# Kernel optimization log

Measured on AMD Instinct MI355X. Metric: run time of the kernel, lower is better.

## Reference

```python
import jax, jax.numpy as jnp
import numpy as np

B, S, H, W, L = 32, 512, 768, 256, 8  # batch, subword seq, hidden, max words, max group size
INTENT, SLOT = 26, 121


def setup_inputs() -> dict:
    key = jax.random.key(0)
    ks = jax.random.split(key, 16)
    sc = 0.02
    res_all = jax.random.normal(ks[0], (B, S, H), jnp.float32)
    res = jax.random.normal(ks[1], (B, H), jnp.float32)
    # group covers indices start..start+lens inclusive (lens+1 <= L elements)
    token_start_idxs = jax.random.randint(ks[2], (B, W), 0, S - L, jnp.int32)
    subword_lengths = jax.random.randint(ks[3], (B, W), 1, L, jnp.int32)  # 1..7
    return {
        'res_all': res_all,
        'res': res,
        'token_start_idxs': token_start_idxs,
        'subword_lengths': subword_lengths,
        'Wsq_w': jax.random.normal(ks[4], (H, H), jnp.float32) * sc,
        'Wsq_b': jnp.zeros((H,), jnp.float32),
        'Wsk_w': jax.random.normal(ks[5], (H, H), jnp.float32) * sc,
        'Wsk_b': jnp.zeros((H,), jnp.float32),
        'Wsv_w': jax.random.normal(ks[6], (H, H), jnp.float32) * sc,
        'Wsv_b': jnp.zeros((H,), jnp.float32),
        'lin_id_w': jax.random.normal(ks[7], (INTENT, H), jnp.float32) * sc,
        'lin_id_b': jnp.zeros((INTENT,), jnp.float32),
        'lin_slot_w': jax.random.normal(ks[8], (SLOT, H), jnp.float32) * sc,
        'lin_slot_b': jnp.zeros((SLOT,), jnp.float32),
    }


def reference(res_all, res, token_start_idxs, subword_lengths,
              Wsq_w, Wsq_b, Wsk_w, Wsk_b, Wsv_w, Wsv_b,
              lin_id_w, lin_id_b, lin_slot_w, lin_slot_b):
    # intent head on pooled output
    res_id = res @ lin_id_w.T + lin_id_b  # [B, INTENT]

    # gather padded subword groups: torch.range is inclusive -> lens+1 subwords
    offs = jnp.arange(L, dtype=jnp.int32)                        # [L]
    idx = token_start_idxs[:, :, None] + offs[None, None, :]     # [B, W, L]
    idx = jnp.clip(idx, 0, S - 1)
    group = res_all[jnp.arange(B)[:, None, None], idx]           # [B, W, L, H]
    valid = offs[None, None, :] <= subword_lengths[:, :, None]   # [B, W, L], lens+1 valid

    # SAA_Attn: only the first row's attention output is used
    q0 = group[:, :, 0, :] @ Wsq_w.T + Wsq_b                     # [B, W, H]
    K = group @ Wsk_w.T + Wsk_b                                  # [B, W, L, H]
    V = group @ Wsv_w.T + Wsv_b                                  # [B, W, L, H]
    scores = jnp.einsum('bwh,bwkh->bwk', q0, K)                  # [B, W, L]
    scores = jnp.where(valid, scores, jnp.float32(-1e9))
    attn = jax.nn.softmax(scores, axis=-1)
    first = group[:, :, 0, :]
    attn_word = jnp.einsum('bwk,bwkh->bwh', attn, V) + first     # [B, W, H]

    # lens == 1 branch bypasses attention entirely
    word = jnp.where((subword_lengths == 1)[:, :, None], first, attn_word)

    res_sf = word @ lin_slot_w.T + lin_slot_b                    # [B, W, SLOT]
    return res_id, res_sf
```

## Files before the change

### kernel.cpp

```cpp
#include <hip/hip_runtime.h>
#include <cstdint>
#include <cstddef>

#define BB 32
#define SS 512
#define HH 768
#define WW 256
#define LL 8
#define NINTENT 26
#define NSLOT 121

typedef float f32x4 __attribute__((ext_vector_type(4)));
typedef __bf16 bf16x8 __attribute__((ext_vector_type(8)));

static __device__ __forceinline__ float bf2f(unsigned short u) {
    union { unsigned int i; float f; } x; x.i = ((unsigned int)u) << 16; return x.f;
}
static __device__ __forceinline__ unsigned short f2bf(float f) {
    union { float f; unsigned int i; } x; x.f = f;
    unsigned int r = (x.i + 0x7fffu + ((x.i >> 16) & 1u)) >> 16;
    return (unsigned short)r;
}

static __device__ __forceinline__ void gload16(const void* g, void* l) {
    __builtin_amdgcn_global_load_lds(
        (const __attribute__((address_space(1))) void*)g,
        (__attribute__((address_space(3))) void*)l, 16, 0, 0);
}

#define MF(a, b, c) __builtin_amdgcn_mfma_f32_16x16x32_bf16((a), (b), (c), 0, 0, 0)

__global__ __launch_bounds__(256) void prep_w(
    const float* __restrict__ Wk, const float* __restrict__ Wq,
    const float* __restrict__ Wv, const float* __restrict__ Ws,
    const float* __restrict__ bq, const float* __restrict__ bv,
    unsigned short* __restrict__ WkT_hi, unsigned short* __restrict__ WkT_lo,
    unsigned short* __restrict__ WqT_hi, unsigned short* __restrict__ WqT_lo,
    unsigned short* __restrict__ WvT, unsigned short* __restrict__ Wcomb,
    float* __restrict__ u_part,
    float* __restrict__ wsbv_part)
{
    int bid = blockIdx.x;
    int t = threadIdx.x;

    if (bid < 432) {
        __shared__ float tl[64][65];
        int mb = bid / 144, tb = bid % 144;
        int tx = tb % 12, ty = tb / 12;
        const float* src = (mb == 0) ? Wk : (mb == 1) ? Wq : Wv;
        int rr = t >> 4, c4 = (t & 15) * 4;
#pragma unroll
        for (int j = 0; j < 4; j++) {
            float4 v = *reinterpret_cast<const float4*>(
                &src[(size_t)(ty * 64 + rr + 16 * j) * HH + tx * 64 + c4]);
            tl[rr + 16 * j][c4 + 0] = v.x; tl[rr + 16 * j][c4 + 1] = v.y;
            tl[rr + 16 * j][c4 + 2] = v.z; tl[rr + 16 * j][c4 + 3] = v.w;
        }
        __syncthreads();
        int il = t >> 4, o4 = (t & 15) * 4;
        unsigned short* dhi = (mb == 0) ? WkT_hi : (mb == 1) ? WqT_hi : WvT;
        unsigned short* dlo = (mb == 0) ? WkT_lo : WqT_lo;
#pragma unroll
        for (int j = 0; j < 4; j++) {
            int i = il + 16 * j;
            float v0 = tl[o4 + 0][i], v1 = tl[o4 + 1][i];
            float v2 = tl[o4 + 2][i], v3 = tl[o4 + 3][i];
            size_t off = (size_t)(tx * 64 + i) * HH + ty * 64 + o4;
            ushort4 h;
            h.x = f2bf(v0); h.y = f2bf(v1); h.z = f2bf(v2); h.w = f2bf(v3);
            *reinterpret_cast<ushort4*>(&dhi[off]) = h;
            if (mb < 2) {
                ushort4 l;
                l.x = f2bf(v0 - bf2f(h.x)); l.y = f2bf(v1 - bf2f(h.y));
                l.z = f2bf(v2 - bf2f(h.z)); l.w = f2bf(v3 - bf2f(h.w));
                *reinterpret_cast<ushort4*>(&dlo[off]) = l;
            }
        }
        if (mb == 0) {
            int c = t >> 2, q = t & 3;
            float s = 0.f;
#pragma unroll
            for (int r = 0; r < 16; r++)
                s += bq[ty * 64 + q * 16 + r] * tl[q * 16 + r][c];
            s += __shfl_xor(s, 1);
            s += __shfl_xor(s, 2);
            if (q == 0) u_part[ty * HH + tx * 64 + c] = s;
        }
    } else {
        __shared__ float wred[4];
        int bid2 = bid - 432;
        int idx = bid2 * 256 + t;
        int row = idx / HH, col = idx % HH;
        float v = (row < NSLOT) ? Ws[row * HH + col] : 0.f;
        Wcomb[row * 1536 + col] = f2bf(v);
        float pv = v * bv[col];
        int lane = t & 63, wave = t >> 6;
#pragma unroll
        for (int off = 32; off > 0; off >>= 1) pv += __shfl_xor(pv, off);
        if (lane == 0) wred[wave] = pv;
        __syncthreads();
        if (t == 0)
            wsbv_part[(bid2 % 3) * 128 + row] = wred[0] + wred[1] + wred[2] + wred[3];
    }
}

__global__ __launch_bounds__(256) void gemm_weights(
    const uint4* __restrict__ WkT_hi, const uint4* __restrict__ WkT_lo,
    const uint4* __restrict__ WqT_hi, const uint4* __restrict__ WqT_lo,
    const uint4* __restrict__ WvT, const uint4* __restrict__ Wcomb,
    const float* __restrict__ res_all, const int* __restrict__ starts,
    const float* __restrict__ res, const float* __restrict__ id_w,
    const float* __restrict__ id_b,
    float* __restrict__ Ppart,
    float* __restrict__ WRpart,
    unsigned short* __restrict__ slotA,
    float* __restrict__ out)
{
    __shared__ uint4 sA[512];
    __shared__ uint4 sB[512];
    int bid = blockIdx.x;
    int t = threadIdx.x;
    int lane = t & 63, wave = t >> 6;

    if (bid >= 2384) {
        int w = (bid - 2384) * 4 + wave;
        int bb = w / 26, o = w - bb * 26;
        const float* rrow = res + bb * HH + lane * 12;
        const float* wrow = id_w + o * HH + lane * 12;
        float s = 0.f;
#pragma unroll
        for (int c = 0; c < 3; c++) {
            float4 a = *reinterpret_cast<const float4*>(&rrow[c * 4]);
            float4 b = *reinterpret_cast<const float4*>(&wrow[c * 4]);
            s += a.x * b.x + a.y * b.y + a.z * b.z + a.w * b.w;
        }
#pragma unroll
        for (int off = 32; off > 0; off >>= 1) s += __shfl_xor(s, off);
        if (lane == 0) out[bb * NINTENT + o] = s + id_b[o];
        return;
    }
    if (bid >= 336) {
        int gw = (bid - 336) * 4 + wave;
        int b = gw >> 8;
        int s0 = starts[gw];
        const float* src = res_all + (size_t)(b * SS + s0) * HH + lane * 12;
        unsigned short* dst = slotA + (size_t)gw * 1536 + lane * 12;
#pragma unroll
        for (int c2 = 0; c2 < 3; c2++) {
            float4 v = *reinterpret_cast<const float4*>(&src[c2 * 4]);
            ushort4 o;
            o.x = f2bf(v.x); o.y = f2bf(v.y); o.z = f2bf(v.z); o.w = f2bf(v.w);
            *reinterpret_cast<ushort4*>(&dst[c2 * 4]) = o;
        }
        return;
    }

    int wm = wave >> 1, wn = wave & 1;
    int l16 = lane & 15, lk = lane >> 4;
    int srow = lane >> 2, schk = lane & 3;
    uint4* sA0 = &sA[wave * 128];
    uint4* sA1 = &sA[wave * 128 + 64];
    uint4* sB0 = &sB[wave * 128];
    uint4* sB1 = &sB[wave * 128 + 64];

    f32x4 acc[4][4] = {};

    if (bid < 288) {
        int tile = bid >> 3, ks = bid & 7;
        int mt = tile / 6, nt = tile % 6;
        int kb = ks * 12;
#pragma unroll
        for (int p = 0; p < 3; p++) {
            const uint4* Ab = (p == 1) ? WkT_lo : WkT_hi;
            const uint4* Bb = (p == 2) ? WqT_lo : WqT_hi;
            const uint4* Ag0 = Ab + (size_t)(mt * 128 + wave * 32 + srow) * 96 + kb + schk;
            const uint4* Ag1 = Ag0 + (size_t)16 * 96;
            const uint4* Bg0 = Bb + (size_t)(nt * 128 + wave * 32 + srow) * 96 + kb + schk;
            const uint4* Bg1 = Bg0 + (size_t)16 * 96;
            for (int k0 = 0; k0 < 12; k0 += 4) {
                gload16(Ag0 + k0, sA0); gload16(Ag1 + k0, sA1);
                gload16(Bg0 + k0, sB0); gload16(Bg1 + k0, sB1);
                __syncthreads();
                bf16x8 af[4], bfr[4];
#pragma unroll
                for (int i = 0; i < 4; i++)
                    af[i] = *reinterpret_cast<const bf16x8*>(&sA[(wm * 64 + i * 16 + l16) * 4 + lk]);
#pragma unroll
                for (int j = 0; j < 4; j++)
                    bfr[j] = *reinterpret_cast<const bf16x8*>(&sB[(wn * 64 + j * 16 + l16) * 4 + lk]);
#pragma unroll
                for (int i = 0; i < 4; i++)
#pragma unroll
                    for (int j = 0; j < 4; j++)
                        acc[i][j] = MF(af[i], bfr[j], acc[i][j]);
                __syncthreads();
            }
        }
        float* dst = Ppart + (size_t)ks * 589824;
#pragma unroll
        for (int i = 0; i < 4; i++)
#pragma unroll
            for (int j = 0; j < 4; j++) {
                int col = nt * 128 + wn * 64 + j * 16 + l16;
#pragma unroll
                for (int q = 0; q < 4; q++) {
                    int row = mt * 128 + wm * 64 + i * 16 + lk * 4 + q;
                    dst[(size_t)row * HH + col] = acc[i][j][q];
                }
            }
    } else {
        int idx = bid - 288;
        int nt = idx >> 3, ks = idx & 7;
        int kb = ks * 12;
        const uint4* Ag0 = Wcomb + (size_t)(wave * 32 + srow) * 192 + kb + schk;
        const uint4* Ag1 = Ag0 + (size_t)16 * 192;
        const uint4* Bg0 = WvT + (size_t)(nt * 128 + wave * 32 + srow) * 96 + kb + schk;
        const uint4* Bg1 = Bg0 + (size_t)16 * 96;
        for (int k0 = 0; k0 < 12; k0 += 4) {
            gload16(Ag0 + k0, sA0); gload16(Ag1 + k0, sA1);
            gload16(Bg0 + k0, sB0); gload16(Bg1 + k0, sB1);
            __syncthreads();
            bf16x8 af[4], bfr[4];
#pragma unroll
            for (int i = 0; i < 4; i++)
                af[i] = *reinterpret_cast<const bf16x8*>(&sA[(wm * 64 + i * 16 + l16) * 4 + lk]);
#pragma unroll
            for (int j = 0; j < 4; j++)
                bfr[j] = *reinterpret_cast<const bf16x8*>(&sB[(wn * 64 + j * 16 + l16) * 4 + lk]);
#pragma unroll
            for (int i = 0; i < 4; i++)
#pragma unroll
                for (int j = 0; j < 4; j++)
                    acc[i][j] = MF(af[i], bfr[j], acc[i][j]);
            __syncthreads();
        }
        float* dst = WRpart + (size_t)ks * 98304;
#pragma unroll
        for (int i = 0; i < 4; i++)
#pragma unroll
            for (int j = 0; j < 4; j++) {
                int col = nt * 128 + wn * 64 + j * 16 + l16;
#pragma unroll
                for (int q = 0; q < 4; q++) {
                    int row = wm * 64 + i * 16 + lk * 4 + q;
                    dst[(size_t)row * HH + col] = acc[i][j][q];
                }
            }
    }
}

__global__ __launch_bounds__(256) void psum_kernel(
    const float4* __restrict__ Ppart, ushort4* __restrict__ Pb,
    const float4* __restrict__ WRpart, unsigned short* __restrict__ Wcomb,
    const float* __restrict__ u_part, float* __restrict__ u,
    const float* __restrict__ wsbv_part, float* __restrict__ wsbv)
{
    int bid = blockIdx.x, t = threadIdx.x;
    if (bid < 576) {
        int i = bid * 256 + t;
        float4 s = Ppart[i];
#pragma unroll
        for (int k = 1; k < 8; k++) {
            float4 v = Ppart[(size_t)k * 147456 + i];
            s.x += v.x; s.y += v.y; s.z += v.z; s.w += v.w;
        }
        ushort4 o;
        o.x = f2bf(s.x); o.y = f2bf(s.y); o.z = f2bf(s.z); o.w = f2bf(s.w);
        Pb[i] = o;
    } else if (bid < 672) {
        int q = (bid - 576) * 256 + t;
        float4 s = WRpart[q];
#pragma unroll
        for (int k = 1; k < 8; k++) {
            float4 v = WRpart[(size_t)k * 24576 + q];
            s.x += v.x; s.y += v.y; s.z += v.z; s.w += v.w;
        }
        int row = q / 192, colq = q % 192;
        ushort4 o;
        o.x = f2bf(s.x); o.y = f2bf(s.y); o.z = f2bf(s.z); o.w = f2bf(s.w);
        *reinterpret_cast<ushort4*>(&Wcomb[row * 1536 + 768 + colq * 4]) = o;
    } else if (bid < 675) {
        int c = (bid - 672) * 256 + t;
        float s = 0.f;
#pragma unroll
        for (int ty = 0; ty < 12; ty++) s += u_part[ty * HH + c];
        u[c] = s;
    } else if (t < 128) {
        wsbv[t] = wsbv_part[t] + wsbv_part[128 + t] + wsbv_part[256 + t];
    }
}

__global__ __launch_bounds__(256) void gemm_qp(
    const uint4* __restrict__ A,
    const uint4* __restrict__ Bm,
    const float* __restrict__ u,
    float* __restrict__ qp)
{
    __shared__ uint4 sA[256];
    __shared__ uint4 sB[512];

    int bid = blockIdx.x;
    bid = (bid & 7) * 96 + (bid >> 3);
    int mt = bid / 6, nt = bid % 6;

    int t = threadIdx.x;
    int lane = t & 63, wave = t >> 6;
    int wm = wave >> 1, wn = wave & 1;
    int l16 = lane & 15, lk = lane >> 4;
    int srow = lane >> 2, schk = lane & 3;

    const uint4* Ag  = A + (size_t)(mt * 64 + wave * 16 + srow) * 192 + schk;
    const uint4* Bg0 = Bm + (size_t)(nt * 128 + wave * 32 + srow) * 96 + schk;
    const uint4* Bg1 = Bg0 + (size_t)16 * 96;
    uint4* sAp = &sA[wave * 64];
    uint4* sB0 = &sB[wave * 128];
    uint4* sB1 = &sB[wave * 128 + 64];

    f32x4 acc[2][4] = {};

    for (int k0 = 0; k0 < 96; k0 += 4) {
        gload16(Ag + k0, sAp);
        gload16(Bg0 + k0, sB0);
        gload16(Bg1 + k0, sB1);
        __syncthreads();
        bf16x8 af[2], bfr[4];
#pragma unroll
        for (int i = 0; i < 2; i++)
            af[i] = *reinterpret_cast<const bf16x8*>(&sA[(wm * 32 + i * 16 + l16) * 4 + lk]);
#pragma unroll
        for (int j = 0; j < 4; j++)
            bfr[j] = *reinterpret_cast<const bf16x8*>(&sB[(wn * 64 + j * 16 + l16) * 4 + lk]);
#pragma unroll
        for (int i = 0; i < 2; i++)
#pragma unroll
            for (int j = 0; j < 4; j++)
                acc[i][j] = MF(af[i], bfr[j], acc[i][j]);
        __syncthreads();
    }

#pragma unroll
    for (int i = 0; i < 2; i++)
#pragma unroll
        for (int j = 0; j < 4; j++) {
            int col = nt * 128 + wn * 64 + j * 16 + l16;
            float add = u[col];
#pragma unroll
            for (int q = 0; q < 4; q++) {
                int row = mt * 64 + wm * 32 + i * 16 + lk * 4 + q;
                qp[(size_t)row * HH + col] = acc[i][j][q] + add;
            }
        }
}

__global__ __launch_bounds__(256) void attn2_kernel(
    const float* __restrict__ qp,
    const float* __restrict__ res_all,
    const int* __restrict__ starts,
    const int* __restrict__ lens,
    unsigned short* __restrict__ slotA)
{
    int bid = blockIdx.x;
    bid = (bid & 7) * 256 + (bid >> 3);
    int gw = bid * 4 + (threadIdx.x >> 6);
    int lane = threadIdx.x & 63;
    int b = gw >> 8;
    int s0 = starts[gw];
    int sl = lens[gw];

    unsigned short* dst = slotA + (size_t)gw * 1536 + 768 + lane * 12;

    if (sl == 1) {
        ushort4 z = {0, 0, 0, 0};
#pragma unroll
        for (int c = 0; c < 3; c++) *reinterpret_cast<ushort4*>(&dst[c * 4]) = z;
        return;
    }

    const float* qrow = qp + (size_t)gw * HH + lane * 12;
    float q[12];
#pragma unroll
    for (int c = 0; c < 3; c++) {
        float4 v = *reinterpret_cast<const float4*>(&qrow[c * 4]);
        q[c * 4 + 0] = v.x; q[c * 4 + 1] = v.y; q[c * 4 + 2] = v.z; q[c * 4 + 3] = v.w;
    }

    float scores[8];
#pragma unroll
    for (int k = 0; k < LL; k++) {
        if (k > sl) break;
        int s = s0 + k; if (s > SS - 1) s = SS - 1;
        const float* xr = res_all + (size_t)(b * SS + s) * HH + lane * 12;
        float partial = 0.f;
#pragma unroll
        for (int c = 0; c < 3; c++) {
            float4 v = *reinterpret_cast<const float4*>(&xr[c * 4]);
            partial += q[c * 4 + 0] * v.x + q[c * 4 + 1] * v.y
                     + q[c * 4 + 2] * v.z + q[c * 4 + 3] * v.w;
        }
#pragma unroll
        for (int off = 32; off > 0; off >>= 1) partial += __shfl_xor(partial, off);
        scores[k] = partial;
    }

    float m = -1e30f;
    for (int k = 0; k < LL; k++) if (k <= sl && scores[k] > m) m = scores[k];
    float p[8], ssum = 0.f;
    for (int k = 0; k < LL; k++) {
        p[k] = (k <= sl) ? __expf(scores[k] - m) : 0.f;
        ssum += p[k];
    }
    float inv = 1.f / ssum;

    float acc[12];
#pragma unroll
    for (int i = 0; i < 12; i++) acc[i] = 0.f;
    for (int k = 0; k < LL; k++) {
        if (k > sl) break;
        int s = s0 + k; if (s > SS - 1) s = SS - 1;
        const float* xr = res_all + (size_t)(b * SS + s) * HH + lane * 12;
        float wk = p[k] * inv;
#pragma unroll
        for (int c = 0; c < 3; c++) {
            float4 v = *reinterpret_cast<const float4*>(&xr[c * 4]);
            acc[c * 4 + 0] += wk * v.x; acc[c * 4 + 1] += wk * v.y;
            acc[c * 4 + 2] += wk * v.z; acc[c * 4 + 3] += wk * v.w;
        }
    }

#pragma unroll
    for (int c = 0; c < 3; c++) {
        ushort4 o;
        o.x = f2bf(acc[c * 4 + 0]); o.y = f2bf(acc[c * 4 + 1]);
        o.z = f2bf(acc[c * 4 + 2]); o.w = f2bf(acc[c * 4 + 3]);
        *reinterpret_cast<ushort4*>(&dst[c * 4]) = o;
    }
}

__global__ __launch_bounds__(256) void gemm_slot3(
    const uint4* __restrict__ A,
    const uint4* __restrict__ Bm,
    float* __restrict__ Cpart)
{
    __shared__ uint4 sA[256];
    __shared__ uint4 sB[512];

    int bid = blockIdx.x;
    int mt = bid >> 1, ks = bid & 1;
    int t = threadIdx.x;
    int lane = t & 63, wave = t >> 6;
    int wm = wave >> 1, wn = wave & 1;
    int l16 = lane & 15, lk = lane >> 4;
    int srow = lane >> 2, schk = lane & 3;

    const uint4* Ag  = A + (size_t)(mt * 64 + wave * 16 + srow) * 192 + ks * 96 + schk;
    const uint4* Bg0 = Bm + (size_t)(wave * 32 + srow) * 192 + ks * 96 + schk;
    const uint4* Bg1 = Bg0 + (size_t)16 * 192;
    uint4* sAp = &sA[wave * 64];
    uint4* sB0 = &sB[wave * 128];
    uint4* sB1 = &sB[wave * 128 + 64];

    f32x4 acc[2][4] = {};

    for (int k0 = 0; k0 < 96; k0 += 4) {
        gload16(Ag + k0, sAp);
        gload16(Bg0 + k0, sB0);
        gload16(Bg1 + k0, sB1);
        __syncthreads();
        bf16x8 af[2], bfr[4];
#pragma unroll
        for (int i = 0; i < 2; i++)
            af[i] = *reinterpret_cast<const bf16x8*>(&sA[(wm * 32 + i * 16 + l16) * 4 + lk]);
#pragma unroll
        for (int j = 0; j < 4; j++)
            bfr[j] = *reinterpret_cast<const bf16x8*>(&sB[(wn * 64 + j * 16 + l16) * 4 + lk]);
#pragma unroll
        for (int i = 0; i < 2; i++)
#pragma unroll
            for (int j = 0; j < 4; j++)
                acc[i][j] = MF(af[i], bfr[j], acc[i][j]);
        __syncthreads();
    }

    float* dst = Cpart + (size_t)ks * 1048576;
#pragma unroll
    for (int i = 0; i < 2; i++)
#pragma unroll
        for (int j = 0; j < 4; j++) {
            int col = wn * 64 + j * 16 + l16;
#pragma unroll
            for (int q = 0; q < 4; q++) {
                int row = mt * 64 + wm * 32 + i * 16 + lk * 4 + q;
                dst[(size_t)row * 128 + col] = acc[i][j][q];
            }
        }
}

__global__ __launch_bounds__(256) void merge_kernel(
    const float* __restrict__ Cpart, const float* __restrict__ bias,
    const float* __restrict__ wsbv, const int* __restrict__ lens,
    float* __restrict__ outsf)
{
    int bid = blockIdx.x, t = threadIdx.x;
    int col = t & 127;
    if (col >= NSLOT) return;
    float bc = bias[col];
    float wv = wsbv[col];
#pragma unroll
    for (int j = 0; j < 2; j++) {
        int row = bid * 4 + (t >> 7) * 2 + j;
        float v = Cpart[(size_t)row * 128 + col]
                + Cpart[(size_t)1048576 + (size_t)row * 128 + col]
                + bc + ((lens[row] > 1) ? wv : 0.f);
        outsf[(size_t)row * NSLOT + col] = v;
    }
}

extern "C" void kernel_launch(void* const* d_in, const int* in_sizes, int n_in,
                              void* d_out, int out_size, void* d_ws, size_t ws_size,
                              hipStream_t stream) {
    const float* res_all    = (const float*)d_in[0];
    const float* res        = (const float*)d_in[1];
    const int*   starts     = (const int*)d_in[2];
    const int*   lens       = (const int*)d_in[3];
    const float* Wsq_w      = (const float*)d_in[4];
    const float* Wsq_b      = (const float*)d_in[5];
    const float* Wsk_w      = (const float*)d_in[6];
    const float* Wsk_b      = (const float*)d_in[7];
    const float* Wsv_w      = (const float*)d_in[8];
    const float* Wsv_b      = (const float*)d_in[9];
    const float* lin_id_w   = (const float*)d_in[10];
    const float* lin_id_b   = (const float*)d_in[11];
    const float* lin_slot_w = (const float*)d_in[12];
    const float* lin_slot_b = (const float*)d_in[13];
    float* out = (float*)d_out;
    (void)Wsk_b;

    char* ws = (char*)d_ws;
    unsigned short* slotA     = (unsigned short*)(ws + 0);
    float*          qp        = (float*)(ws + 25165824);
    unsigned short* WkT_hi    = (unsigned short*)(ws + 50331648);
    unsigned short* WkT_lo    = (unsigned short*)(ws + 51511296);
    unsigned short* WqT_hi    = (unsigned short*)(ws + 52690944);
    unsigned short* WqT_lo    = (unsigned short*)(ws + 53870592);
    unsigned short* WvT       = (unsigned short*)(ws + 55050240);
    unsigned short* Pb        = (unsigned short*)(ws + 56229888);
    unsigned short* Wcomb     = (unsigned short*)(ws + 57409536);
    float*          u         = (float*)(ws + 57802752);
    float*          wsbv      = (float*)(ws + 57805824);
    float*          u_part    = (float*)(ws + 57806336);
    float*          wsbv_part = (float*)(ws + 57843200);
    float*          Ppart     = (float*)(ws + 57845760);
    float*          WRpart    = (float*)(ws + 76720128);
    float*          Cpart     = (float*)(ws + 79865856);

    prep_w<<<816, 256, 0, stream>>>(
        Wsk_w, Wsq_w, Wsv_w, lin_slot_w, Wsq_b, Wsv_b,
        WkT_hi, WkT_lo, WqT_hi, WqT_lo, WvT, Wcomb,
        u_part, wsbv_part);

    gemm_weights<<<2592, 256, 0, stream>>>(
        (const uint4*)WkT_hi, (const uint4*)WkT_lo,
        (const uint4*)WqT_hi, (const uint4*)WqT_lo,
        (const uint4*)WvT, (const uint4*)Wcomb,
        res_all, starts, res, lin_id_w, lin_id_b,
        Ppart, WRpart, slotA, out);

    psum_kernel<<<676, 256, 0, stream>>>(
        (const float4*)Ppart, (ushort4*)Pb, (const float4*)WRpart, Wcomb,
        u_part, u, wsbv_part, wsbv);

    gemm_qp<<<768, 256, 0, stream>>>((const uint4*)slotA, (const uint4*)Pb, u, qp);

    attn2_kernel<<<2048, 256, 0, stream>>>(qp, res_all, starts, lens, slotA);

    gemm_slot3<<<256, 256, 0, stream>>>((const uint4*)slotA, (const uint4*)Wcomb, Cpart);

    merge_kernel<<<2048, 256, 0, stream>>>(Cpart, lin_slot_b, wsbv, lens, out + 832);
}
```

Measured before the change: 97.49 us.

## Move first-half slot GEMM into qp kernel, fuse merge into epilogue, online softmax

The first K-half of the slot GEMM only needs the gathered first-token features, so it now runs as 256 extra blocks inside the qp GEMM launch and writes Cpart0. The second K-half kernel, which depends on the attention output, reads Cpart0 and adds bias and wsbv in its epilogue, which removes the separate merge kernel and one launch. The attention kernel switches to a single-pass online softmax, so each res_all row is read once instead of twice. This adds per-step exp rescaling, and the slot GEMM tiles shrink to 32 rows, which lowers MFMA reuse per block.

```diff
diff --git a/kernel.cpp b/kernel.cpp
--- a/kernel.cpp
+++ b/kernel.cpp
@@ -290,24 +290,62 @@
     }
 }
 
-__global__ __launch_bounds__(256) void gemm_qp(
+__global__ __launch_bounds__(256) void gemm_qp_sl(
     const uint4* __restrict__ A,
     const uint4* __restrict__ Bm,
+    const uint4* __restrict__ Wc,
     const float* __restrict__ u,
-    float* __restrict__ qp)
+    float* __restrict__ qp,
+    float* __restrict__ Cpart0)
 {
     __shared__ uint4 sA[256];
     __shared__ uint4 sB[512];
 
     int bid = blockIdx.x;
-    bid = (bid & 7) * 96 + (bid >> 3);
-    int mt = bid / 6, nt = bid % 6;
-
     int t = threadIdx.x;
     int lane = t & 63, wave = t >> 6;
     int wm = wave >> 1, wn = wave & 1;
     int l16 = lane & 15, lk = lane >> 4;
     int srow = lane >> 2, schk = lane & 3;
+
+    if (bid >= 768) {
+        int mt = bid - 768;
+        const uint4* Ag  = A + (size_t)(mt * 32 + wave * 16 + srow) * 192 + schk;
+        const uint4* Bg0 = Wc + (size_t)(wave * 32 + srow) * 192 + schk;
+        const uint4* Bg1 = Bg0 + (size_t)16 * 192;
+        uint4* sB0 = &sB[wave * 128];
+        uint4* sB1 = &sB[wave * 128 + 64];
+
+        f32x4 acc[4] = {};
+        for (int k0 = 0; k0 < 96; k0 += 4) {
+            if (wave < 2) gload16(Ag + k0, &sA[wave * 64]);
+            gload16(Bg0 + k0, sB0);
+            gload16(Bg1 + k0, sB1);
+            __syncthreads();
+            bf16x8 af = *reinterpret_cast<const bf16x8*>(&sA[(wm * 16 + l16) * 4 + lk]);
+            bf16x8 bfr[4];
+#pragma unroll
+            for (int j = 0; j < 4; j++)
+                bfr[j] = *reinterpret_cast<const bf16x8*>(&sB[(wn * 64 + j * 16 + l16) * 4 + lk]);
+#pragma unroll
+            for (int j = 0; j < 4; j++)
+                acc[j] = MF(af, bfr[j], acc[j]);
+            __syncthreads();
+        }
+#pragma unroll
+        for (int j = 0; j < 4; j++) {
+            int col = wn * 64 + j * 16 + l16;
+#pragma unroll
+            for (int q = 0; q < 4; q++) {
+                int row = mt * 32 + wm * 16 + lk * 4 + q;
+                Cpart0[(size_t)row * 128 + col] = acc[j][q];
+            }
+        }
+        return;
+    }
+
+    bid = (bid & 7) * 96 + (bid >> 3);
+    int mt = bid / 6, nt = bid % 6;
 
     const uint4* Ag  = A + (size_t)(mt * 64 + wave * 16 + srow) * 192 + schk;
     const uint4* Bg0 = Bm + (size_t)(nt * 128 + wave * 32 + srow) * 96 + schk;
@@ -384,134 +422,102 @@
         q[c * 4 + 0] = v.x; q[c * 4 + 1] = v.y; q[c * 4 + 2] = v.z; q[c * 4 + 3] = v.w;
     }
 
-    float scores[8];
-#pragma unroll
+    float m = -1e30f, ssum = 0.f;
+    float acc[12];
+#pragma unroll
+    for (int i = 0; i < 12; i++) acc[i] = 0.f;
+
     for (int k = 0; k < LL; k++) {
         if (k > sl) break;
         int s = s0 + k; if (s > SS - 1) s = SS - 1;
         const float* xr = res_all + (size_t)(b * SS + s) * HH + lane * 12;
+        float x[12];
         float partial = 0.f;
 #pragma unroll
         for (int c = 0; c < 3; c++) {
             float4 v = *reinterpret_cast<const float4*>(&xr[c * 4]);
+            x[c * 4 + 0] = v.x; x[c * 4 + 1] = v.y;
+            x[c * 4 + 2] = v.z; x[c * 4 + 3] = v.w;
             partial += q[c * 4 + 0] * v.x + q[c * 4 + 1] * v.y
                      + q[c * 4 + 2] * v.z + q[c * 4 + 3] * v.w;
         }
 #pragma unroll
         for (int off = 32; off > 0; off >>= 1) partial += __shfl_xor(partial, off);
-        scores[k] = partial;
-    }
-
-    float m = -1e30f;
-    for (int k = 0; k < LL; k++) if (k <= sl && scores[k] > m) m = scores[k];
-    float p[8], ssum = 0.f;
-    for (int k = 0; k < LL; k++) {
-        p[k] = (k <= sl) ? __expf(scores[k] - m) : 0.f;
-        ssum += p[k];
-    }
+
+        float mnew = (partial > m) ? partial : m;
+        float scale = __expf(m - mnew);
+        float e = __expf(partial - mnew);
+        ssum = ssum * scale + e;
+#pragma unroll
+        for (int i = 0; i < 12; i++) acc[i] = acc[i] * scale + e * x[i];
+        m = mnew;
+    }
+
     float inv = 1.f / ssum;
-
-    float acc[12];
-#pragma unroll
-    for (int i = 0; i < 12; i++) acc[i] = 0.f;
-    for (int k = 0; k < LL; k++) {
-        if (k > sl) break;
-        int s = s0 + k; if (s > SS - 1) s = SS - 1;
-        const float* xr = res_all + (size_t)(b * SS + s) * HH + lane * 12;
-        float wk = p[k] * inv;
-#pragma unroll
-        for (int c = 0; c < 3; c++) {
-            float4 v = *reinterpret_cast<const float4*>(&xr[c * 4]);
-            acc[c * 4 + 0] += wk * v.x; acc[c * 4 + 1] += wk * v.y;
-            acc[c * 4 + 2] += wk * v.z; acc[c * 4 + 3] += wk * v.w;
-        }
-    }
-
 #pragma unroll
     for (int c = 0; c < 3; c++) {
         ushort4 o;
-        o.x = f2bf(acc[c * 4 + 0]); o.y = f2bf(acc[c * 4 + 1]);
-        o.z = f2bf(acc[c * 4 + 2]); o.w = f2bf(acc[c * 4 + 3]);
+        o.x = f2bf(acc[c * 4 + 0] * inv); o.y = f2bf(acc[c * 4 + 1] * inv);
+        o.z = f2bf(acc[c * 4 + 2] * inv); o.w = f2bf(acc[c * 4 + 3] * inv);
         *reinterpret_cast<ushort4*>(&dst[c * 4]) = o;
     }
 }
 
-__global__ __launch_bounds__(256) void gemm_slot3(
+__global__ __launch_bounds__(256) void gemm_slot_r(
     const uint4* __restrict__ A,
     const uint4* __restrict__ Bm,
-    float* __restrict__ Cpart)
+    const float* __restrict__ Cpart0,
+    const float* __restrict__ bias, const float* __restrict__ wsbv,
+    const int* __restrict__ lens,
+    float* __restrict__ outsf)
 {
-    __shared__ uint4 sA[256];
+    __shared__ uint4 sA[128];
     __shared__ uint4 sB[512];
 
-    int bid = blockIdx.x;
-    int mt = bid >> 1, ks = bid & 1;
+    int mt = blockIdx.x;
     int t = threadIdx.x;
     int lane = t & 63, wave = t >> 6;
     int wm = wave >> 1, wn = wave & 1;
     int l16 = lane & 15, lk = lane >> 4;
     int srow = lane >> 2, schk = lane & 3;
 
-    const uint4* Ag  = A + (size_t)(mt * 64 + wave * 16 + srow) * 192 + ks * 96 + schk;
-    const uint4* Bg0 = Bm + (size_t)(wave * 32 + srow) * 192 + ks * 96 + schk;
+    const uint4* Ag  = A + (size_t)(mt * 32 + wave * 16 + srow) * 192 + 96 + schk;
+    const uint4* Bg0 = Bm + (size_t)(wave * 32 + srow) * 192 + 96 + schk;
     const uint4* Bg1 = Bg0 + (size_t)16 * 192;
-    uint4* sAp = &sA[wave * 64];
     uint4* sB0 = &sB[wave * 128];
     uint4* sB1 = &sB[wave * 128 + 64];
 
-    f32x4 acc[2][4] = {};
+    f32x4 acc[4] = {};
 
     for (int k0 = 0; k0 < 96; k0 += 4) {
-        gload16(Ag + k0, sAp);
+        if (wave < 2) gload16(Ag + k0, &sA[wave * 64]);
         gload16(Bg0 + k0, sB0);
         gload16(Bg1 + k0, sB1);
         __syncthreads();
-        bf16x8 af[2], bfr[4];
-#pragma unroll
-        for (int i = 0; i < 2; i++)
-            af[i] = *reinterpret_cast<const bf16x8*>(&sA[(wm * 32 + i * 16 + l16) * 4 + lk]);
+        bf16x8 af = *reinterpret_cast<const bf16x8*>(&sA[(wm * 16 + l16) * 4 + lk]);
+        bf16x8 bfr[4];
 #pragma unroll
         for (int j = 0; j < 4; j++)
             bfr[j] = *reinterpret_cast<const bf16x8*>(&sB[(wn * 64 + j * 16 + l16) * 4 + lk]);
 #pragma unroll
-        for (int i = 0; i < 2; i++)
-#pragma unroll
-            for (int j = 0; j < 4; j++)
-                acc[i][j] = MF(af[i], bfr[j], acc[i][j]);
+        for (int j = 0; j < 4; j++)
+            acc[j] = MF(af, bfr[j], acc[j]);
         __syncthreads();
     }
 
-    float* dst = Cpart + (size_t)ks * 1048576;
-#pragma unroll
-    for (int i = 0; i < 2; i++)
-#pragma unroll
-        for (int j = 0; j < 4; j++) {
-            int col = wn * 64 + j * 16 + l16;
+#pragma unroll
+    for (int j = 0; j < 4; j++) {
+        int col = wn * 64 + j * 16 + l16;
+        if (col < NSLOT) {
+            float bc = bias[col], wv = wsbv[col];
 #pragma unroll
             for (int q = 0; q < 4; q++) {
-                int row = mt * 64 + wm * 32 + i * 16 + lk * 4 + q;
-                dst[(size_t)row * 128 + col] = acc[i][j][q];
-            }
-        }
-}
-
-__global__ __launch_bounds__(256) void merge_kernel(
-    const float* __restrict__ Cpart, const float* __restrict__ bias,
-    const float* __restrict__ wsbv, const int* __restrict__ lens,
-    float* __restrict__ outsf)
-{
-    int bid = blockIdx.x, t = threadIdx.x;
-    int col = t & 127;
-    if (col >= NSLOT) return;
-    float bc = bias[col];
-    float wv = wsbv[col];
-#pragma unroll
-    for (int j = 0; j < 2; j++) {
-        int row = bid * 4 + (t >> 7) * 2 + j;
-        float v = Cpart[(size_t)row * 128 + col]
-                + Cpart[(size_t)1048576 + (size_t)row * 128 + col]
-                + bc + ((lens[row] > 1) ? wv : 0.f);
-        outsf[(size_t)row * NSLOT + col] = v;
+                int row = mt * 32 + wm * 16 + lk * 4 + q;
+                float v = acc[j][q] + Cpart0[(size_t)row * 128 + col]
+                        + bc + ((lens[row] > 1) ? wv : 0.f);
+                outsf[(size_t)row * NSLOT + col] = v;
+            }
+        }
     }
 }
 
@@ -551,7 +557,7 @@
     float*          wsbv_part = (float*)(ws + 57843200);
     float*          Ppart     = (float*)(ws + 57845760);
     float*          WRpart    = (float*)(ws + 76720128);
-    float*          Cpart     = (float*)(ws + 79865856);
+    float*          Cpart0    = (float*)(ws + 79865856);
 
     prep_w<<<816, 256, 0, stream>>>(
         Wsk_w, Wsq_w, Wsv_w, lin_slot_w, Wsq_b, Wsv_b,
@@ -569,11 +575,11 @@
         (const float4*)Ppart, (ushort4*)Pb, (const float4*)WRpart, Wcomb,
         u_part, u, wsbv_part, wsbv);
 
-    gemm_qp<<<768, 256, 0, stream>>>((const uint4*)slotA, (const uint4*)Pb, u, qp);
+    gemm_qp_sl<<<1024, 256, 0, stream>>>((const uint4*)slotA, (const uint4*)Pb,
+                                         (const uint4*)Wcomb, u, qp, Cpart0);
 
     attn2_kernel<<<2048, 256, 0, stream>>>(qp, res_all, starts, lens, slotA);
 
-    gemm_slot3<<<256, 256, 0, stream>>>((const uint4*)slotA, (const uint4*)Wcomb, Cpart);
-
-    merge_kernel<<<2048, 256, 0, stream>>>(Cpart, lin_slot_b, wsbv, lens, out + 832);
-}
+    gemm_slot_r<<<256, 256, 0, stream>>>((const uint4*)slotA, (const uint4*)Wcomb,
+                                         Cpart0, lin_slot_b, wsbv, lens, out + 832);
+}
```

New measurement: 88.31 us. 1.1x faster.
